# Optimization experiments

Measured on AMD Instinct MI355X. Metric: run time of the kernel, lower is better.

## Reference

```python
import jax, jax.numpy as jnp
import numpy as np

MAP_W = 500
INTERP_H, INTERP_W = 1024, 2048


def _bilinear_ac(x, out_h, out_w):
    # torch F.interpolate(mode='bilinear', align_corners=True), separable
    N, C, H, W = x.shape
    ys = jnp.linspace(0.0, H - 1, out_h)
    y0 = jnp.floor(ys).astype(jnp.int32)
    y1 = jnp.minimum(y0 + 1, H - 1)
    wy = (ys - y0.astype(x.dtype))[None, None, :, None]
    rows = x[:, :, y0, :] * (1 - wy) + x[:, :, y1, :] * wy  # (N,C,out_h,W)
    xs = jnp.linspace(0.0, W - 1, out_w)
    x0 = jnp.floor(xs).astype(jnp.int32)
    x1 = jnp.minimum(x0 + 1, W - 1)
    wx = (xs - x0.astype(x.dtype))[None, None, None, :]
    return rows[:, :, :, x0] * (1 - wx) + rows[:, :, :, x1] * wx


def _conv(x, w, pad):
    return jax.lax.conv_general_dilated(x, w, (1, 1), [(pad, pad), (pad, pad)],
                                        dimension_numbers=('NCHW', 'OIHW', 'NCHW'))


def _bn_relu(x, g, b):
    # BatchNorm2d in training mode: biased batch stats over (N,H,W)
    mu = jnp.mean(x, axis=(0, 2, 3), keepdims=True)
    var = jnp.var(x, axis=(0, 2, 3), keepdims=True)
    xn = (x - mu) * jax.lax.rsqrt(var + 1e-5)
    return jax.nn.relu(xn * g[None, :, None, None] + b[None, :, None, None])


def setup_inputs() -> dict:
    key = jax.random.key(0)
    ks = jax.random.split(key, 24)
    C, NOBJ = 64, 21
    features = jax.random.normal(ks[0], (1, 1, C, 256, 512), dtype=jnp.float32)
    proj_indices = jax.random.randint(ks[1], (1, MAP_W * MAP_W), 0, 400000, dtype=jnp.int64)
    masks_inliers = jax.random.bernoulli(ks[2], 0.5, (1, INTERP_H, INTERP_W))
    rgb_no_norm = jax.random.uniform(ks[3], (1, INTERP_H, INTERP_W, 3), dtype=jnp.float32) * 255.0
    def cw(k, o, i, kh, kw):
        return jax.random.normal(k, (o, i, kh, kw), dtype=jnp.float32) * (1.0 / np.sqrt(i * kh * kw))
    return {
        'features': features, 'proj_indices': proj_indices,
        'masks_inliers': masks_inliers, 'rgb_no_norm': rgb_no_norm,
        'w1': cw(ks[4], 128, C, 7, 7), 'g1': jnp.ones(128), 'b1': jnp.zeros(128),
        'w2': cw(ks[5], 64, 128, 3, 3), 'g2': jnp.ones(64), 'b2': jnp.zeros(64),
        'w3': cw(ks[6], 48, 64, 3, 3), 'g3': jnp.ones(48), 'b3': jnp.zeros(48),
        'w4': cw(ks[7], 48, 48, 3, 3), 'g4': jnp.ones(48), 'b4': jnp.zeros(48),
        'w5': cw(ks[8], NOBJ, 48, 1, 1), 'b5': jnp.zeros(NOBJ),
    }


def reference(features, proj_indices, masks_inliers, rgb_no_norm,
              w1, g1, b1, w2, g2, b2, w3, g3, b3, w4, g4, b4, w5, b5):
    N, T, C, H, W = features.shape  # N = 1
    feat = _bilinear_ac(features[:, 0], INTERP_H, INTERP_W)      # (N,C,1024,2048)
    feat = feat.transpose(0, 2, 3, 1).reshape(-1, C)             # row-major NHWC flatten
    rgb_flat = rgb_no_norm.reshape(-1, 3)
    mask_flat = masks_inliers.reshape(-1)
    # stable compaction: inlier pixels first, in original row-major order
    # (equivalent to torch boolean-mask gather feature[mask_inliers, :])
    order = jnp.argsort((~mask_flat).astype(jnp.int32), stable=True)
    compact_f = feat[order]
    compact_rgb = rgb_flat[order]
    idx = proj_indices.reshape(-1)
    m = idx < jnp.max(idx)                                       # sentinel = max value
    state = jnp.where(m[:, None], compact_f[idx], 0.0)           # replace-mode scatter
    state_rgb = jnp.where(m[:, None], compact_rgb[idx], 0.0)
    rgb_write = state_rgb.reshape(MAP_W, MAP_W, 3)
    observed_masks = m.reshape(N, MAP_W, MAP_W)
    memory = state.reshape(N, MAP_W, MAP_W, C).transpose(0, 3, 1, 2)
    # decoder (first conv in_channels fixed to C to match memory)
    x = _bn_relu(_conv(memory, w1, 3), g1, b1)
    x = _bn_relu(_conv(x, w2, 1), g2, b2)
    x = _bn_relu(_conv(x, w3, 1), g3, b3)
    x = _bn_relu(_conv(x, w4, 1), g4, b4)
    semmap = _conv(x, w5, 0) + b5[None, :, None, None]
    return (semmap, observed_masks, rgb_write)
```

## Files before the change

kernel.cpp:

```cpp
#include <hip/hip_runtime.h>

#define MAPN 250000
#define NPIX 2097152

typedef unsigned short ushort_t;
typedef __attribute__((ext_vector_type(4))) float f32x4;

__device__ inline ushort_t f2bf(float f){
  unsigned u = __float_as_uint(f);
  u = (u + 0x7fffu + ((u >> 16) & 1u)) >> 16;
  return (ushort_t)u;
}
__device__ inline float bf2f(ushort_t h){ return __uint_as_float(((unsigned)h) << 16); }

__device__ __forceinline__ void glds16(const void* g, void* l){
  __builtin_amdgcn_global_load_lds((const __attribute__((address_space(1))) unsigned int*)g,
                                   (__attribute__((address_space(3))) unsigned int*)l, 16, 0, 0);
}

__device__ inline int read_mask(const void* p, int i, int t){
  if (t==0) return ((const int*)p)[i] != 0;
  if (t==1) return ((const unsigned char*)p)[i] != 0;
  if (t==3) return ((const long long*)p)[i] != 0;
  return ((const float*)p)[i] != 0.0f;
}
__device__ inline int read_idx(const void* p, int i, int t){
  if (t==1) return (int)((const long long*)p)[i];
  return ((const int*)p)[i];
}

__global__ void detect_kernel(const int* __restrict__ mask_w, const int* __restrict__ idx_w,
                              int* __restrict__ flags, int* __restrict__ maxidx){
  int tid = threadIdx.x;
  int orv=0, modd=0, inz=0;
  for (int i=tid;i<4096;i+=256) orv |= mask_w[i];
  for (int i=tid;i<2048;i+=256) modd += (mask_w[2*i+1]!=0);
  for (int i=tid;i<2048;i+=256) inz  += (idx_w[2*i+1]!=0);
  __shared__ int sOr[256], sM[256], sI[256];
  sOr[tid]=orv; sM[tid]=modd; sI[tid]=inz; __syncthreads();
  for (int o=128;o;o>>=1){ if(tid<o){ sOr[tid]|=sOr[tid+o]; sM[tid]+=sM[tid+o]; sI[tid]+=sI[tid+o]; } __syncthreads(); }
  if (tid==0){
    int o = sOr[0];
    int mt;
    if ((o & ~1) == 0)               mt = (sM[0] > 0) ? 0 : 3;
    else if ((o & ~0x01010101) == 0) mt = 1;
    else                             mt = 2;
    flags[0] = mt;
    flags[1] = (sI[0] > 0) ? 0 : 1;
    maxidx[0] = 0;
  }
}

__global__ void feat_transpose(const float* __restrict__ f, ushort_t* __restrict__ out){
  __shared__ float tile[64][65];
  int tid = threadIdx.x;
  int y = blockIdx.y;
  int x0 = blockIdx.x * 64;
  #pragma unroll
  for (int pass=0; pass<16; pass++){
    int c = pass*4 + (tid>>6);
    int x = x0 + (tid & 63);
    tile[c][tid & 63] = f[(size_t)c*131072 + (size_t)y*512 + x];
  }
  __syncthreads();
  #pragma unroll
  for (int pass=0; pass<16; pass++){
    int xl = pass*4 + (tid>>6);
    int c  = tid & 63;
    out[((size_t)y*512 + x0 + xl)*64 + c] = f2bf(tile[c][xl]);
  }
}

__global__ void scan_count(const void* __restrict__ mask, const int* __restrict__ flags,
                           int* __restrict__ blkSums){
  int t = flags[0];
  int tid = threadIdx.x;
  int base = blockIdx.x*1024 + tid*4;
  int s = 0;
  #pragma unroll
  for (int j=0;j<4;j++) s += read_mask(mask, base+j, t);
  __shared__ int red[256];
  red[tid] = s; __syncthreads();
  for (int o=128;o;o>>=1){ if (tid<o) red[tid]+=red[tid+o]; __syncthreads(); }
  if (tid==0) blkSums[blockIdx.x] = red[0];
}

__global__ void scan_offsets(const int* __restrict__ blkSums, int* __restrict__ blkOffs){
  __shared__ int tsum[256];
  int tid = threadIdx.x;
  int loc[8]; int s=0;
  #pragma unroll
  for (int j=0;j<8;j++){ loc[j]=blkSums[tid*8+j]; s+=loc[j]; }
  tsum[tid]=s; __syncthreads();
  for (int o=1;o<256;o<<=1){
    int v = (tid>=o)? tsum[tid-o] : 0;
    __syncthreads();
    tsum[tid] += v;
    __syncthreads();
  }
  int run = tsum[tid]-s;
  #pragma unroll
  for (int j=0;j<8;j++){ blkOffs[tid*8+j]=run; run+=loc[j]; }
  if (tid==255) blkOffs[2048]=run;
}

__global__ void build_table(const void* __restrict__ mask, const int* __restrict__ flags,
                            const int* __restrict__ blkOffs, int* __restrict__ table){
  int t = flags[0];
  int tid = threadIdx.x;
  int base = blockIdx.x*1024 + tid*4;
  int mv[4]; int s=0;
  #pragma unroll
  for (int j=0;j<4;j++){ mv[j]=read_mask(mask, base+j, t); s+=mv[j]; }
  __shared__ int red[256];
  red[tid]=s; __syncthreads();
  for (int o=1;o<256;o<<=1){
    int v = (tid>=o)? red[tid-o] : 0;
    __syncthreads();
    red[tid]+=v;
    __syncthreads();
  }
  int excl = red[tid]-s + blkOffs[blockIdx.x];
  int total = blkOffs[2048];
  #pragma unroll
  for (int j=0;j<4;j++){
    int p = base+j;
    int pos;
    if (mv[j]){ pos = excl; excl++; }
    else      { pos = total + (p - excl); }
    table[pos] = p;
  }
}

__global__ void max_idx_kernel(const void* __restrict__ idxp, const int* __restrict__ flags,
                               int* __restrict__ mx){
  int t = flags[1];
  int m = 0;
  for (int i = blockIdx.x*blockDim.x + threadIdx.x; i < MAPN; i += gridDim.x*blockDim.x)
    m = max(m, read_idx(idxp, i, t));
  #pragma unroll
  for (int o=32;o;o>>=1) m = max(m, __shfl_down(m, o));
  if ((threadIdx.x & 63) == 0) atomicMax(mx, m);
}

__global__ void gather_kernel(const void* __restrict__ idxp, const int* __restrict__ flags,
                              const int* __restrict__ mxp, const int* __restrict__ table,
                              const ushort_t* __restrict__ Fhwc, const float* __restrict__ rgb,
                              unsigned char* __restrict__ mem_f8, float* __restrict__ out_obs,
                              float* __restrict__ out_rgb){
  int cell = blockIdx.x*4 + (threadIdx.x>>6);
  int lane = threadIdx.x & 63;
  int t = flags[1];
  int mx = *mxp;
  int idx = read_idx(idxp, cell, t);
  bool m = idx < mx;
  float v = 0.0f, r = 0.0f;
  if (m){
    int p = table[idx];
    int py = p >> 11, px = p & 2047;
    float fy = py * (255.0f/1023.0f);
    int y0 = (int)fy; float wy = fy - (float)y0; int y1 = min(y0+1, 255);
    float fx = px * (511.0f/2047.0f);
    int x0 = (int)fx; float wx = fx - (float)x0; int x1 = min(x0+1, 511);
    const ushort_t* f00 = Fhwc + ((size_t)y0*512 + x0)*64;
    const ushort_t* f01 = Fhwc + ((size_t)y0*512 + x1)*64;
    const ushort_t* f10 = Fhwc + ((size_t)y1*512 + x0)*64;
    const ushort_t* f11 = Fhwc + ((size_t)y1*512 + x1)*64;
    float w00=(1.0f-wy)*(1.0f-wx), w01=(1.0f-wy)*wx, w10=wy*(1.0f-wx), w11=wy*wx;
    v = w00*bf2f(f00[lane]) + w01*bf2f(f01[lane]) + w10*bf2f(f10[lane]) + w11*bf2f(f11[lane]);
    if (lane < 3) r = rgb[(size_t)p*3 + lane];
  }
  int q = __builtin_amdgcn_cvt_pk_fp8_f32(v, 0.0f, 0, false);
  mem_f8[(size_t)cell*64 + lane] = (unsigned char)(q & 0xff);
  if (lane == 0) out_obs[cell] = m ? 1.0f : 0.0f;
  if (lane < 3)  out_rgb[(size_t)cell*3 + lane] = r;
}

__device__ void wprep_body(const float* __restrict__ w, unsigned char* __restrict__ out,
                           int O, int I, int CIPAD, int KK, int co){
  int n = KK*CIPAD;
  int NFS = (O+15)>>4;
  int KC  = CIPAD>>5;
  float mx = 0.f;
  for (int e=threadIdx.x; e<n; e+=256){
    int ci = e % CIPAD;
    if (ci < I){
      int t = e / CIPAD;
      mx = fmaxf(mx, fabsf(w[((size_t)co*I + ci)*KK + t]));
    }
  }
  __shared__ float red[256];
  red[threadIdx.x]=mx; __syncthreads();
  for (int o=128;o;o>>=1){ if(threadIdx.x<o) red[threadIdx.x]=fmaxf(red[threadIdx.x],red[threadIdx.x+o]); __syncthreads(); }
  float m = red[0];
  float sc = (m > 0.f) ? exp2f(floorf(log2f(224.0f/m))) : 1.0f;
  for (int e=threadIdx.x; e<n; e+=256){
    int t = e / CIPAD, ci = e % CIPAD;
    float v = (ci < I) ? w[((size_t)co*I + ci)*KK + t]*sc : 0.0f;
    int q = __builtin_amdgcn_cvt_pk_fp8_f32(v, 0.0f, 0, false);
    int kc = ci>>5, g=(ci>>3)&3, j=ci&7;
    int l = g*16 + (co&15);
    size_t pos = ((size_t)(t*KC + kc)*NFS + (co>>4))*512 + l*8 + j;
    out[pos] = (unsigned char)(q & 0xff);
  }
}

__global__ void wprep_all(const float* __restrict__ w1, unsigned char* __restrict__ o1,
                          const float* __restrict__ w2, unsigned char* __restrict__ o2,
                          const float* __restrict__ w3, unsigned char* __restrict__ o3,
                          const float* __restrict__ w4, unsigned char* __restrict__ o4){
  int b = blockIdx.x;
  if      (b < 128) wprep_body(w1, o1, 128, 64, 64, 49, b);
  else if (b < 192) wprep_body(w2, o2, 64, 128, 128, 9, b-128);
  else if (b < 240) wprep_body(w3, o3, 48, 64, 64, 9, b-192);
  else              wprep_body(w4, o4, 48, 48, 64, 9, b-240);
}

template<int CI, int CO, int COPAD, int KS, int PAD, bool HASBN, int CIREAL,
         int TR, int WM, int WN>
__global__ __launch_bounds__(256, 2) void conv2d_f8(const void* __restrict__ in,
                                                    const unsigned char* __restrict__ wt,
                                                    const float* __restrict__ scsh,
                                                    ushort_t* __restrict__ out,
                                                    float* __restrict__ partials){
  constexpr int TCOL = 64;
  constexpr int ECOL = TCOL + 2*PAD;
  constexpr int E    = TR*ECOL;
  constexpr int MF   = TR*4;
  constexpr int MI   = MF/WM;
  constexpr int NFS  = CO/16;
  constexpr int NFW  = NFS/WN;
  constexpr int KC   = CI/32;
  constexpr int CIG  = CI/8;
  constexpr int TB   = CO*CI;
  constexpr int NSL  = TB/1024;
  constexpr int TOT  = E*CIG;
  constexpr int PASSES = (TOT+255)/256;
  constexpr int SCN = HASBN ? CIREAL : 1;

  __shared__ unsigned char sA[E*CI + 128];
  __shared__ unsigned char sB[KS*TB];
  __shared__ float sStat[4][NFW][16][2];
  __shared__ float sSc[SCN], sSh[SCN];

  const int tid = threadIdx.x, lane = tid & 63, wv = tid >> 6;
  const int wm = wv / WN, wn = wv % WN;
  const int cc = blockIdx.x & 7;
  const int rb = blockIdx.x >> 3;
  const int x0 = cc*TCOL, yb = rb*TR;

  const ushort_t* inb = (const ushort_t*)in;
  const unsigned char* in8 = (const unsigned char*)in;

  if (HASBN){
    for (int i=tid;i<CIREAL;i+=256){ sSc[i]=scsh[i]; sSh[i]=scsh[CIREAL+i]; }
    __syncthreads();
  }

  int ebase[MI], frow[MI], fcolb[MI];
  #pragma unroll
  for (int mi=0;mi<MI;mi++){
    int f = wm*MI + mi;
    frow[mi]  = f >> 2;
    fcolb[mi] = (f & 3) * 16;
    ebase[mi] = frow[mi]*ECOL + fcolb[mi] + (lane & 15);
  }

  f32x4 acc[MI][NFW];
  #pragma unroll
  for (int mi=0;mi<MI;mi++)
    #pragma unroll
    for (int ni=0;ni<NFW;ni++) acc[mi][ni] = (f32x4)0.0f;

  if constexpr (!HASBN){
    uint2 areg[PASSES];
    #pragma unroll
    for (int i=0;i<PASSES;i++){
      int c = i*256 + tid;
      uint2 q = make_uint2(0u,0u);
      if ((TOT % 256 == 0) || c < TOT){
        int e = c / CIG, ci8 = (c % CIG)*8;
        int row = e / ECOL, col = e % ECOL;
        int yy = yb + row - PAD;
        int xx = x0 + col - PAD;
        if (((unsigned)yy < 500u) && ((unsigned)xx < 500u))
          q = *(const uint2*)(in8 + ((size_t)yy*500 + xx)*CI + ci8);
      }
      areg[i] = q;
    }
    for (int kh=0; kh<KS; kh++){
      #pragma unroll
      for (int i=0;i<PASSES;i++){
        int c = i*256 + tid;
        if ((TOT % 256 == 0) || c < TOT){
          int e = c / CIG, ci8 = (c % CIG)*8;
          unsigned wa = ((unsigned)(e*CI + ci8)) ^ ((unsigned)(e&15)<<3);
          *(uint2*)(sA + wa) = areg[i];
        }
      }
      {
        const char* wsrc = (const char*)wt + (size_t)kh*KS*TB;
        for (int s=wv; s<KS*NSL; s+=4)
          glds16(wsrc + (size_t)s*1024 + lane*16, &sB[s*1024]);
      }
      __syncthreads();
      if (kh+1 < KS){
        #pragma unroll
        for (int i=0;i<PASSES;i++){
          int c = i*256 + tid;
          uint2 q = make_uint2(0u,0u);
          if ((TOT % 256 == 0) || c < TOT){
            int e = c / CIG, ci8 = (c % CIG)*8;
            int row = e / ECOL, col = e % ECOL;
            int yy = yb + row + (kh+1) - PAD;
            int xx = x0 + col - PAD;
            if (((unsigned)yy < 500u) && ((unsigned)xx < 500u))
              q = *(const uint2*)(in8 + ((size_t)yy*500 + xx)*CI + ci8);
          }
          areg[i] = q;
        }
      }
      for (int kw=0; kw<KS; kw++){
        const unsigned char* bb = sB + kw*TB;
        #pragma unroll
        for (int kc=0;kc<KC;kc++){
          long long bfr[NFW];
          #pragma unroll
          for (int ni=0;ni<NFW;ni++)
            bfr[ni] = *(const long long*)(bb + (((kc*NFS + wn*NFW + ni)<<9) + lane*8));
          #pragma unroll
          for (int mi=0;mi<MI;mi++){
            int e = ebase[mi] + kw;
            unsigned ra = ((unsigned)(e*CI + kc*32 + (lane>>4)*8)) ^ ((unsigned)(e&15)<<3);
            long long af = *(const long long*)(sA + ra);
            #pragma unroll
            for (int ni=0;ni<NFW;ni++)
              acc[mi][ni] = __builtin_amdgcn_mfma_f32_16x16x32_fp8_fp8(af, bfr[ni], acc[mi][ni], 0,0,0);
          }
        }
      }
      __syncthreads();
    }
  } else {
    for (int kh=0; kh<KS; kh++){
      #pragma unroll
      for (int i=0;i<PASSES;i++){
        int c = i*256 + tid;
        if ((TOT % 256 == 0) || c < TOT){
          int e = c / CIG, ci8 = (c % CIG)*8;
          int row = e / ECOL, col = e % ECOL;
          int yy = yb + row + kh - PAD;
          int xx = x0 + col - PAD;
          uint2 q = make_uint2(0u,0u);
          bool ok = ((unsigned)yy < 500u) && ((unsigned)xx < 500u) && (ci8 < CIREAL);
          if (ok){
            uint4 v = *(const uint4*)(inb + ((size_t)yy*500 + xx)*CI + ci8);
            ushort_t* hv = (ushort_t*)&v;
            float f[8];
            #pragma unroll
            for (int j=0;j<8;j++)
              f[j] = fmaxf(fmaf(bf2f(hv[j]), sSc[ci8+j], sSh[ci8+j]), 0.0f);
            int d0 = __builtin_amdgcn_cvt_pk_fp8_f32(f[0], f[1], 0, false);
            d0     = __builtin_amdgcn_cvt_pk_fp8_f32(f[2], f[3], d0, true);
            int d1 = __builtin_amdgcn_cvt_pk_fp8_f32(f[4], f[5], 0, false);
            d1     = __builtin_amdgcn_cvt_pk_fp8_f32(f[6], f[7], d1, true);
            q = make_uint2((unsigned)d0, (unsigned)d1);
          }
          unsigned wa = ((unsigned)(e*CI + ci8)) ^ ((unsigned)(e&15)<<3);
          *(uint2*)(sA + wa) = q;
        }
      }
      {
        const char* wsrc = (const char*)wt + (size_t)kh*KS*TB;
        for (int s=wv; s<KS*NSL; s+=4)
          glds16(wsrc + (size_t)s*1024 + lane*16, &sB[s*1024]);
      }
      __syncthreads();

      for (int kw=0; kw<KS; kw++){
        const unsigned char* bb = sB + kw*TB;
        #pragma unroll
        for (int kc=0;kc<KC;kc++){
          long long bfr[NFW];
          #pragma unroll
          for (int ni=0;ni<NFW;ni++)
            bfr[ni] = *(const long long*)(bb + (((kc*NFS + wn*NFW + ni)<<9) + lane*8));
          #pragma unroll
          for (int mi=0;mi<MI;mi++){
            int e = ebase[mi] + kw;
            unsigned ra = ((unsigned)(e*CI + kc*32 + (lane>>4)*8)) ^ ((unsigned)(e&15)<<3);
            long long af = *(const long long*)(sA + ra);
            #pragma unroll
            for (int ni=0;ni<NFW;ni++)
              acc[mi][ni] = __builtin_amdgcn_mfma_f32_16x16x32_fp8_fp8(af, bfr[ni], acc[mi][ni], 0,0,0);
          }
        }
      }
      __syncthreads();
    }
  }

  #pragma unroll
  for (int ni=0;ni<NFW;ni++){
    float ps=0.f, pq=0.f;
    #pragma unroll
    for (int mi=0;mi<MI;mi++){
      int colb = fcolb[mi] + (lane>>4)*4;
      size_t rowoff = (size_t)(yb + frow[mi])*500;
      #pragma unroll
      for (int j=0;j<4;j++){
        float v = acc[mi][ni][j];
        int colAbs = x0 + colb + j;
        if (colAbs < 500){
          ps += v; pq += v*v;
          out[(rowoff + colAbs)*COPAD + wn*(NFW*16) + ni*16 + (lane&15)] = f2bf(v);
        }
      }
    }
    ps += __shfl_xor(ps, 16); pq += __shfl_xor(pq, 16);
    ps += __shfl_xor(ps, 32); pq += __shfl_xor(pq, 32);
    if (lane < 16){ sStat[wv][ni][lane][0]=ps; sStat[wv][ni][lane][1]=pq; }
  }
  __syncthreads();
  if (tid < CO){
    int wn_ = tid / (NFW*16);
    int r = tid % (NFW*16);
    int ni_ = r >> 4, col = r & 15;
    float s = 0.f, q = 0.f;
    #pragma unroll
    for (int m=0;m<WM;m++){
      s += sStat[m*WN + wn_][ni_][col][0];
      q += sStat[m*WN + wn_][ni_][col][1];
    }
    partials[(size_t)blockIdx.x*(2*CO) + tid]      = s;
    partials[(size_t)blockIdx.x*(2*CO) + CO + tid] = q;
  }
}

__global__ void bn_reduce2(const float* __restrict__ partials, int nblk, int CO,
                           const float* __restrict__ g, const float* __restrict__ b,
                           float* __restrict__ scsh){
  int c = blockIdx.x;
  float s=0.f, q=0.f;
  for (int i=threadIdx.x; i<nblk; i+=256){
    s += partials[(size_t)i*(2*CO) + c];
    q += partials[(size_t)i*(2*CO) + CO + c];
  }
  __shared__ float rs[256], rq[256];
  rs[threadIdx.x]=s; rq[threadIdx.x]=q; __syncthreads();
  for (int o=128;o;o>>=1){
    if (threadIdx.x<o){ rs[threadIdx.x]+=rs[threadIdx.x+o]; rq[threadIdx.x]+=rq[threadIdx.x+o]; }
    __syncthreads();
  }
  if (threadIdx.x==0){
    float mean = rs[0]*(1.0f/(float)MAPN);
    float var  = rq[0]*(1.0f/(float)MAPN) - mean*mean;
    float inv  = rsqrtf(var + 1e-5f);
    float sc   = g[c]*inv;
    scsh[c]    = sc;
    scsh[CO+c] = b[c] - mean*sc;
  }
}

__global__ void conv5_kernel(const ushort_t* __restrict__ in, const float* __restrict__ w,
                             const float* __restrict__ bias, const float* __restrict__ scsh,
                             float* __restrict__ out){
  __shared__ float sw[21*48];
  __shared__ float sb[21];
  __shared__ float sc[48], sh[48];
  for (int i=threadIdx.x;i<1008;i+=256) sw[i]=w[i];
  if (threadIdx.x<21) sb[threadIdx.x]=bias[threadIdx.x];
  if (threadIdx.x<48){ sc[threadIdx.x]=scsh[threadIdx.x]; sh[threadIdx.x]=scsh[48+threadIdx.x]; }
  __syncthreads();
  int pix = blockIdx.x*256 + threadIdx.x;
  if (pix >= MAPN) return;
  float acc[21];
  #pragma unroll
  for (int i=0;i<21;i++) acc[i]=0.0f;
  const ushort_t* ip = in + (size_t)pix*64;
  #pragma unroll
  for (int cg=0; cg<6; cg++){
    uint4 v = *(const uint4*)(ip + cg*8);
    ushort_t* hv = (ushort_t*)&v;
    #pragma unroll
    for (int j=0;j<8;j++){
      int ci = cg*8+j;
      float s = fmaxf(fmaf(bf2f(hv[j]), sc[ci], sh[ci]), 0.0f);
      #pragma unroll
      for (int co=0;co<21;co++) acc[co]=fmaf(s, sw[co*48+ci], acc[co]);
    }
  }
  #pragma unroll
  for (int co=0;co<21;co++) out[(size_t)co*MAPN + pix] = acc[co] + sb[co];
}

static inline size_t al256(size_t x){ return (x + 255) & ~(size_t)255; }

extern "C" void kernel_launch(void* const* d_in, const int* in_sizes, int n_in,
                              void* d_out, int out_size, void* d_ws, size_t ws_size,
                              hipStream_t stream){
  const float* features = (const float*)d_in[0];
  const void*  proj     = d_in[1];
  const void*  mask     = d_in[2];
  const float* rgb      = (const float*)d_in[3];
  const float* w1 = (const float*)d_in[4];
  const float* g1 = (const float*)d_in[5];
  const float* b1 = (const float*)d_in[6];
  const float* w2 = (const float*)d_in[7];
  const float* g2 = (const float*)d_in[8];
  const float* b2 = (const float*)d_in[9];
  const float* w3 = (const float*)d_in[10];
  const float* g3 = (const float*)d_in[11];
  const float* b3 = (const float*)d_in[12];
  const float* w4 = (const float*)d_in[13];
  const float* g4 = (const float*)d_in[14];
  const float* b4 = (const float*)d_in[15];
  const float* w5 = (const float*)d_in[16];
  const float* b5 = (const float*)d_in[17];

  char* ws = (char*)d_ws;
  size_t off = 0;
  unsigned char* mem_f8 = (unsigned char*)(ws + off); off += al256((size_t)MAPN*64);
  ushort_t* actA   = (ushort_t*)(ws + off); off += al256((size_t)MAPN*128*2);
  ushort_t* actB   = (ushort_t*)(ws + off); off += al256((size_t)MAPN*64*2);
  ushort_t* Fhwc   = (ushort_t*)(ws + off); off += al256((size_t)131072*64*2);
  int*      table  = (int*)(ws + off);      off += al256((size_t)NPIX*4);
  unsigned char* wh1 = (unsigned char*)(ws + off); off += al256((size_t)49*64*128);
  unsigned char* wh2 = (unsigned char*)(ws + off); off += al256((size_t)9*128*64);
  unsigned char* wh3 = (unsigned char*)(ws + off); off += al256((size_t)9*64*48);
  unsigned char* wh4 = (unsigned char*)(ws + off); off += al256((size_t)9*64*48);
  float*    partials = (float*)(ws + off);  off += al256((size_t)2048*256*4);
  int* blkSums = (int*)(ws + off); off += al256(2048*4);
  int* blkOffs = (int*)(ws + off); off += al256(2049*4);
  int* maxidx  = (int*)(ws + off); off += 256;
  int* flags   = (int*)(ws + off); off += 256;
  float* scsh1 = (float*)(ws + off); off += al256(256*4);
  float* scsh2 = (float*)(ws + off); off += al256(256*4);
  float* scsh3 = (float*)(ws + off); off += al256(256*4);
  float* scsh4 = (float*)(ws + off); off += al256(256*4);

  float* out_sem = (float*)d_out;
  float* out_obs = out_sem + (size_t)21*MAPN;
  float* out_rgb = out_obs + MAPN;

  detect_kernel<<<1,256,0,stream>>>((const int*)mask, (const int*)proj, flags, maxidx);
  feat_transpose<<<dim3(8,256),256,0,stream>>>(features, Fhwc);

  scan_count<<<2048,256,0,stream>>>(mask, flags, blkSums);
  scan_offsets<<<1,256,0,stream>>>(blkSums, blkOffs);
  build_table<<<2048,256,0,stream>>>(mask, flags, blkOffs, table);

  max_idx_kernel<<<256,256,0,stream>>>(proj, flags, maxidx);

  wprep_all<<<288,256,0,stream>>>(w1, wh1, w2, wh2, w3, wh3, w4, wh4);

  gather_kernel<<<62500,256,0,stream>>>(proj, flags, maxidx, table, Fhwc, rgb,
                                        mem_f8, out_obs, out_rgb);

  conv2d_f8<64,128,128,7,3,false,64,4,2,2><<<125*8,256,0,stream>>>(mem_f8, wh1, nullptr, actA, partials);
  bn_reduce2<<<128,256,0,stream>>>(partials, 1000, 128, g1, b1, scsh1);

  conv2d_f8<128,64,64,3,1,true,128,4,2,2><<<125*8,256,0,stream>>>(actA, wh2, scsh1, actB, partials);
  bn_reduce2<<<64,256,0,stream>>>(partials, 1000, 64, g2, b2, scsh2);

  conv2d_f8<64,48,64,3,1,true,64,4,4,1><<<125*8,256,0,stream>>>(actB, wh3, scsh2, actA, partials);
  bn_reduce2<<<48,256,0,stream>>>(partials, 1000, 48, g3, b3, scsh3);

  conv2d_f8<64,48,64,3,1,true,48,4,4,1><<<125*8,256,0,stream>>>(actA, wh4, scsh3, actB, partials);
  bn_reduce2<<<48,256,0,stream>>>(partials, 1000, 48, g4, b4, scsh4);

  conv5_kernel<<<(MAPN+255)/256,256,0,stream>>>(actB, w5, b5, scsh4, out_sem);
}
```

Before: 422.2 us.

## Use 16x16x128 scaled MFMA for 7x7 conv1 with split output channels

Replaces the generic fp8 conv for the first 7x7 layer with a dedicated kernel using the larger-K mfma_scale 16x16x128 f8f6f4 instruction. Pairs of kw taps are packed into the 128-wide K dimension, with zero padding for the odd tap, and the weights are re-laid out by a new prep kernel. Output channels are split across a second grid dimension (2x64), which doubles the block count and shrinks per-block weight shared memory. The costs are one wasted zero-padded K slice per row and a new BN partial-reduction kernel matching the split layout.

New measurement: 946.7 us. 124% more time.

```diff
diff --git a/kernel.cpp b/kernel.cpp
--- a/kernel.cpp
+++ b/kernel.cpp
@@ -5,6 +5,9 @@
 
 typedef unsigned short ushort_t;
 typedef __attribute__((ext_vector_type(4))) float f32x4;
+typedef __attribute__((ext_vector_type(8))) int int8v;
+
+union U8 { long long q[4]; int8v v; };
 
 __device__ inline ushort_t f2bf(float f){
   unsigned u = __float_as_uint(f);
@@ -176,6 +179,37 @@
   if (lane < 3)  out_rgb[(size_t)cell*3 + lane] = r;
 }
 
+__global__ void wprep1_mx(const float* __restrict__ w, unsigned char* __restrict__ out){
+  int co = blockIdx.x;
+  float mx = 0.f;
+  for (int e=threadIdx.x; e<3136; e+=256){
+    int ci = e & 63, t = e >> 6;
+    mx = fmaxf(mx, fabsf(w[((size_t)co*64 + ci)*49 + t]));
+  }
+  __shared__ float red[256];
+  red[threadIdx.x]=mx; __syncthreads();
+  for (int o=128;o;o>>=1){ if(threadIdx.x<o) red[threadIdx.x]=fmaxf(red[threadIdx.x],red[threadIdx.x+o]); __syncthreads(); }
+  float m = red[0];
+  float sc = (m > 0.f) ? exp2f(floorf(log2f(224.0f/m))) : 1.0f;
+  int nf = co>>4, zz = nf>>2, nfz = nf&3;
+  for (int e=threadIdx.x; e<3136; e+=256){
+    int ci = e & 63, t = e >> 6;
+    int kh = t/7, kw = t - kh*7;
+    float v = w[((size_t)co*64 + ci)*49 + t]*sc;
+    int q = __builtin_amdgcn_cvt_pk_fp8_f32(v, 0.0f, 0, false);
+    int p = kw>>1, k = ((kw&1)<<6) | ci;
+    int ln = (k>>5)*16 + (co&15), j = k&31;
+    size_t pos = ((size_t)((kh*2 + zz)*4 + p)*4 + nfz)*2048 + (j>>3)*512 + ln*8 + (j&7);
+    out[pos] = (unsigned char)(q & 0xff);
+  }
+  for (int e=threadIdx.x; e<448; e+=256){
+    int kh = e>>6; int k = 64 + (e&63);
+    int ln = (k>>5)*16 + (co&15), j = k&31;
+    size_t pos = ((size_t)((kh*2 + zz)*4 + 3)*4 + nfz)*2048 + (j>>3)*512 + ln*8 + (j&7);
+    out[pos] = 0;
+  }
+}
+
 __device__ void wprep_body(const float* __restrict__ w, unsigned char* __restrict__ out,
                            int O, int I, int CIPAD, int KK, int co){
   int n = KK*CIPAD;
@@ -205,19 +239,181 @@
   }
 }
 
-__global__ void wprep_all(const float* __restrict__ w1, unsigned char* __restrict__ o1,
-                          const float* __restrict__ w2, unsigned char* __restrict__ o2,
+__global__ void wprep_all(const float* __restrict__ w2, unsigned char* __restrict__ o2,
                           const float* __restrict__ w3, unsigned char* __restrict__ o3,
                           const float* __restrict__ w4, unsigned char* __restrict__ o4){
   int b = blockIdx.x;
-  if      (b < 128) wprep_body(w1, o1, 128, 64, 64, 49, b);
-  else if (b < 192) wprep_body(w2, o2, 64, 128, 128, 9, b-128);
-  else if (b < 240) wprep_body(w3, o3, 48, 64, 64, 9, b-192);
-  else              wprep_body(w4, o4, 48, 48, 64, 9, b-240);
-}
-
-template<int CI, int CO, int COPAD, int KS, int PAD, bool HASBN, int CIREAL,
-         int TR, int WM, int WN>
+  if      (b < 64)  wprep_body(w2, o2, 64, 128, 128, 9, b);
+  else if (b < 112) wprep_body(w3, o3, 48, 64, 64, 9, b-64);
+  else              wprep_body(w4, o4, 48, 48, 64, 9, b-112);
+}
+
+__global__ __launch_bounds__(256, 2) void conv1_mx(const unsigned char* __restrict__ in8,
+                                                   const unsigned char* __restrict__ wt,
+                                                   ushort_t* __restrict__ out,
+                                                   float* __restrict__ partials){
+  constexpr int ECOL = 70, E = 280, CIG = 8, TOT = E*CIG, PASSES = 9;
+  __shared__ unsigned char sA[E*64 + 128];
+  __shared__ unsigned char sB[32768];
+  __shared__ float sStat[4][2][16][2];
+
+  const int tid = threadIdx.x, lane = tid & 63, wv = tid >> 6;
+  const int wm = wv >> 1, wn = wv & 1;
+  const int cc = blockIdx.x & 7, rb = blockIdx.x >> 3;
+  const int z = blockIdx.y;
+  const int x0 = cc*64, yb = rb*4;
+
+  int ebase[8], frow[8], fcolb[8];
+  #pragma unroll
+  for (int mi=0;mi<8;mi++){
+    int f = wm*8 + mi;
+    frow[mi]  = f >> 2;
+    fcolb[mi] = (f & 3) * 16;
+    ebase[mi] = frow[mi]*ECOL + fcolb[mi] + (lane & 15);
+  }
+
+  f32x4 acc[8][2];
+  #pragma unroll
+  for (int mi=0;mi<8;mi++){ acc[mi][0]=(f32x4)0.0f; acc[mi][1]=(f32x4)0.0f; }
+
+  uint2 areg[PASSES];
+  #pragma unroll
+  for (int i=0;i<PASSES;i++){
+    int c = i*256 + tid;
+    uint2 q = make_uint2(0u,0u);
+    if (c < TOT){
+      int e = c / CIG, ci8 = (c % CIG)*8;
+      int row = e / ECOL, col = e % ECOL;
+      int yy = yb + row - 3, xx = x0 + col - 3;
+      if (((unsigned)yy < 500u) && ((unsigned)xx < 500u))
+        q = *(const uint2*)(in8 + ((size_t)yy*500 + xx)*64 + ci8);
+    }
+    areg[i] = q;
+  }
+
+  for (int kh=0; kh<7; kh++){
+    #pragma unroll
+    for (int i=0;i<PASSES;i++){
+      int c = i*256 + tid;
+      if (c < TOT){
+        int e = c / CIG, ci8 = (c % CIG)*8;
+        unsigned wa = ((unsigned)(e*64 + ci8)) ^ ((unsigned)(e&15)<<3);
+        *(uint2*)(sA + wa) = areg[i];
+      }
+    }
+    {
+      const char* wsrc = (const char*)wt + (size_t)(kh*2 + z)*32768;
+      for (int s=wv; s<32; s+=4)
+        glds16(wsrc + (size_t)s*1024 + lane*16, &sB[s*1024]);
+    }
+    __syncthreads();
+    if (kh+1 < 7){
+      #pragma unroll
+      for (int i=0;i<PASSES;i++){
+        int c = i*256 + tid;
+        uint2 q = make_uint2(0u,0u);
+        if (c < TOT){
+          int e = c / CIG, ci8 = (c % CIG)*8;
+          int row = e / ECOL, col = e % ECOL;
+          int yy = yb + row + (kh+1) - 3, xx = x0 + col - 3;
+          if (((unsigned)yy < 500u) && ((unsigned)xx < 500u))
+            q = *(const uint2*)(in8 + ((size_t)yy*500 + xx)*64 + ci8);
+        }
+        areg[i] = q;
+      }
+    }
+    #pragma unroll
+    for (int p=0;p<4;p++){
+      U8 b0, b1;
+      {
+        unsigned bb0 = (unsigned)((p*4 + wn*2 + 0)*2048) + lane*8;
+        unsigned bb1 = (unsigned)((p*4 + wn*2 + 1)*2048) + lane*8;
+        b0.q[0]=*(const long long*)(sB+bb0);      b0.q[1]=*(const long long*)(sB+bb0+512);
+        b0.q[2]=*(const long long*)(sB+bb0+1024); b0.q[3]=*(const long long*)(sB+bb0+1536);
+        b1.q[0]=*(const long long*)(sB+bb1);      b1.q[1]=*(const long long*)(sB+bb1+512);
+        b1.q[2]=*(const long long*)(sB+bb1+1024); b1.q[3]=*(const long long*)(sB+bb1+1536);
+      }
+      #pragma unroll
+      for (int mi=0;mi<8;mi++){
+        int e = ebase[mi] + 2*p + ((lane>>5)&1);
+        unsigned ab = (unsigned)(e*64 + ((lane>>4)&1)*32);
+        unsigned sw = (unsigned)((e&15)<<3);
+        U8 a;
+        a.q[0]=*(const long long*)(sA + ((ab   )^sw));
+        a.q[1]=*(const long long*)(sA + ((ab+ 8)^sw));
+        a.q[2]=*(const long long*)(sA + ((ab+16)^sw));
+        a.q[3]=*(const long long*)(sA + ((ab+24)^sw));
+        acc[mi][0] = __builtin_amdgcn_mfma_scale_f32_16x16x128_f8f6f4(
+                       a.v, b0.v, acc[mi][0], 0, 0, 0, 0x7f7f7f7f, 0, 0x7f7f7f7f);
+        acc[mi][1] = __builtin_amdgcn_mfma_scale_f32_16x16x128_f8f6f4(
+                       a.v, b1.v, acc[mi][1], 0, 0, 0, 0x7f7f7f7f, 0, 0x7f7f7f7f);
+      }
+    }
+    __syncthreads();
+  }
+
+  #pragma unroll
+  for (int ni=0;ni<2;ni++){
+    float ps=0.f, pq=0.f;
+    #pragma unroll
+    for (int mi=0;mi<8;mi++){
+      int colb = fcolb[mi] + (lane>>4)*4;
+      size_t rowoff = (size_t)(yb + frow[mi])*500;
+      #pragma unroll
+      for (int j=0;j<4;j++){
+        float v = acc[mi][ni][j];
+        int colAbs = x0 + colb + j;
+        if (colAbs < 500){
+          ps += v; pq += v*v;
+          out[(rowoff + colAbs)*128 + z*64 + wn*32 + ni*16 + (lane&15)] = f2bf(v);
+        }
+      }
+    }
+    ps += __shfl_xor(ps, 16); pq += __shfl_xor(pq, 16);
+    ps += __shfl_xor(ps, 32); pq += __shfl_xor(pq, 32);
+    if (lane < 16){ sStat[wv][ni][lane][0]=ps; sStat[wv][ni][lane][1]=pq; }
+  }
+  __syncthreads();
+  if (tid < 64){
+    int wn_ = tid >> 5;
+    int r = tid & 31;
+    int ni_ = r >> 4, col = r & 15;
+    float s = sStat[0*2+wn_][ni_][col][0] + sStat[1*2+wn_][ni_][col][0];
+    float q = sStat[0*2+wn_][ni_][col][1] + sStat[1*2+wn_][ni_][col][1];
+    size_t row = (size_t)z*1000 + blockIdx.x;
+    partials[row*128 + tid]      = s;
+    partials[row*128 + 64 + tid] = q;
+  }
+}
+
+__global__ void bn_reduce_l1(const float* __restrict__ partials,
+                             const float* __restrict__ g, const float* __restrict__ b,
+                             float* __restrict__ scsh){
+  int c = blockIdx.x;
+  int zz = c >> 6, cc = c & 63;
+  const float* base = partials + (size_t)zz*1000*128;
+  float s=0.f, q=0.f;
+  for (int i=threadIdx.x; i<1000; i+=256){
+    s += base[(size_t)i*128 + cc];
+    q += base[(size_t)i*128 + 64 + cc];
+  }
+  __shared__ float rs[256], rq[256];
+  rs[threadIdx.x]=s; rq[threadIdx.x]=q; __syncthreads();
+  for (int o=128;o;o>>=1){
+    if (threadIdx.x<o){ rs[threadIdx.x]+=rs[threadIdx.x+o]; rq[threadIdx.x]+=rq[threadIdx.x+o]; }
+    __syncthreads();
+  }
+  if (threadIdx.x==0){
+    float mean = rs[0]*(1.0f/(float)MAPN);
+    float var  = rq[0]*(1.0f/(float)MAPN) - mean*mean;
+    float inv  = rsqrtf(var + 1e-5f);
+    float sc   = g[c]*inv;
+    scsh[c]     = sc;
+    scsh[128+c] = b[c] - mean*sc;
+  }
+}
+
+template<int CI, int CO, int COPAD, int KS, int PAD, int CIREAL, int TR, int WM, int WN>
 __global__ __launch_bounds__(256, 2) void conv2d_f8(const void* __restrict__ in,
                                                     const unsigned char* __restrict__ wt,
                                                     const float* __restrict__ scsh,
@@ -236,12 +432,11 @@
   constexpr int NSL  = TB/1024;
   constexpr int TOT  = E*CIG;
   constexpr int PASSES = (TOT+255)/256;
-  constexpr int SCN = HASBN ? CIREAL : 1;
 
   __shared__ unsigned char sA[E*CI + 128];
   __shared__ unsigned char sB[KS*TB];
   __shared__ float sStat[4][NFW][16][2];
-  __shared__ float sSc[SCN], sSh[SCN];
+  __shared__ float sSc[CIREAL], sSh[CIREAL];
 
   const int tid = threadIdx.x, lane = tid & 63, wv = tid >> 6;
   const int wm = wv / WN, wn = wv % WN;
@@ -250,12 +445,9 @@
   const int x0 = cc*TCOL, yb = rb*TR;
 
   const ushort_t* inb = (const ushort_t*)in;
-  const unsigned char* in8 = (const unsigned char*)in;
-
-  if (HASBN){
-    for (int i=tid;i<CIREAL;i+=256){ sSc[i]=scsh[i]; sSh[i]=scsh[CIREAL+i]; }
-    __syncthreads();
-  }
+
+  for (int i=tid;i<CIREAL;i+=256){ sSc[i]=scsh[i]; sSh[i]=scsh[CIREAL+i]; }
+  __syncthreads();
 
   int ebase[MI], frow[MI], fcolb[MI];
   #pragma unroll
@@ -272,132 +464,61 @@
     #pragma unroll
     for (int ni=0;ni<NFW;ni++) acc[mi][ni] = (f32x4)0.0f;
 
-  if constexpr (!HASBN){
-    uint2 areg[PASSES];
+  for (int kh=0; kh<KS; kh++){
     #pragma unroll
     for (int i=0;i<PASSES;i++){
       int c = i*256 + tid;
-      uint2 q = make_uint2(0u,0u);
       if ((TOT % 256 == 0) || c < TOT){
         int e = c / CIG, ci8 = (c % CIG)*8;
         int row = e / ECOL, col = e % ECOL;
-        int yy = yb + row - PAD;
+        int yy = yb + row + kh - PAD;
         int xx = x0 + col - PAD;
-        if (((unsigned)yy < 500u) && ((unsigned)xx < 500u))
-          q = *(const uint2*)(in8 + ((size_t)yy*500 + xx)*CI + ci8);
-      }
-      areg[i] = q;
-    }
-    for (int kh=0; kh<KS; kh++){
+        uint2 q = make_uint2(0u,0u);
+        bool ok = ((unsigned)yy < 500u) && ((unsigned)xx < 500u) && (ci8 < CIREAL);
+        if (ok){
+          uint4 v = *(const uint4*)(inb + ((size_t)yy*500 + xx)*CI + ci8);
+          ushort_t* hv = (ushort_t*)&v;
+          float f[8];
+          #pragma unroll
+          for (int j=0;j<8;j++)
+            f[j] = fmaxf(fmaf(bf2f(hv[j]), sSc[ci8+j], sSh[ci8+j]), 0.0f);
+          int d0 = __builtin_amdgcn_cvt_pk_fp8_f32(f[0], f[1], 0, false);
+          d0     = __builtin_amdgcn_cvt_pk_fp8_f32(f[2], f[3], d0, true);
+          int d1 = __builtin_amdgcn_cvt_pk_fp8_f32(f[4], f[5], 0, false);
+          d1     = __builtin_amdgcn_cvt_pk_fp8_f32(f[6], f[7], d1, true);
+          q = make_uint2((unsigned)d0, (unsigned)d1);
+        }
+        unsigned wa = ((unsigned)(e*CI + ci8)) ^ ((unsigned)(e&15)<<3);
+        *(uint2*)(sA + wa) = q;
+      }
+    }
+    {
+      const char* wsrc = (const char*)wt + (size_t)kh*KS*TB;
+      for (int s=wv; s<KS*NSL; s+=4)
+        glds16(wsrc + (size_t)s*1024 + lane*16, &sB[s*1024]);
+    }
+    __syncthreads();
+
+    for (int kw=0; kw<KS; kw++){
+      const unsigned char* bb = sB + kw*TB;
       #pragma unroll
-      for (int i=0;i<PASSES;i++){
-        int c = i*256 + tid;
-        if ((TOT % 256 == 0) || c < TOT){
-          int e = c / CIG, ci8 = (c % CIG)*8;
-          unsigned wa = ((unsigned)(e*CI + ci8)) ^ ((unsigned)(e&15)<<3);
-          *(uint2*)(sA + wa) = areg[i];
-        }
-      }
-      {
-        const char* wsrc = (const char*)wt + (size_t)kh*KS*TB;
-        for (int s=wv; s<KS*NSL; s+=4)
-          glds16(wsrc + (size_t)s*1024 + lane*16, &sB[s*1024]);
-      }
-      __syncthreads();
-      if (kh+1 < KS){
+      for (int kc=0;kc<KC;kc++){
+        long long bfr[NFW];
         #pragma unroll
-        for (int i=0;i<PASSES;i++){
-          int c = i*256 + tid;
-          uint2 q = make_uint2(0u,0u);
-          if ((TOT % 256 == 0) || c < TOT){
-            int e = c / CIG, ci8 = (c % CIG)*8;
-            int row = e / ECOL, col = e % ECOL;
-            int yy = yb + row + (kh+1) - PAD;
-            int xx = x0 + col - PAD;
-            if (((unsigned)yy < 500u) && ((unsigned)xx < 500u))
-              q = *(const uint2*)(in8 + ((size_t)yy*500 + xx)*CI + ci8);
-          }
-          areg[i] = q;
-        }
-      }
-      for (int kw=0; kw<KS; kw++){
-        const unsigned char* bb = sB + kw*TB;
+        for (int ni=0;ni<NFW;ni++)
+          bfr[ni] = *(const long long*)(bb + (((kc*NFS + wn*NFW + ni)<<9) + lane*8));
         #pragma unroll
-        for (int kc=0;kc<KC;kc++){
-          long long bfr[NFW];
+        for (int mi=0;mi<MI;mi++){
+          int e = ebase[mi] + kw;
+          unsigned ra = ((unsigned)(e*CI + kc*32 + (lane>>4)*8)) ^ ((unsigned)(e&15)<<3);
+          long long af = *(const long long*)(sA + ra);
           #pragma unroll
           for (int ni=0;ni<NFW;ni++)
-            bfr[ni] = *(const long long*)(bb + (((kc*NFS + wn*NFW + ni)<<9) + lane*8));
-          #pragma unroll
-          for (int mi=0;mi<MI;mi++){
-            int e = ebase[mi] + kw;
-            unsigned ra = ((unsigned)(e*CI + kc*32 + (lane>>4)*8)) ^ ((unsigned)(e&15)<<3);
-            long long af = *(const long long*)(sA + ra);
-            #pragma unroll
-            for (int ni=0;ni<NFW;ni++)
-              acc[mi][ni] = __builtin_amdgcn_mfma_f32_16x16x32_fp8_fp8(af, bfr[ni], acc[mi][ni], 0,0,0);
-          }
+            acc[mi][ni] = __builtin_amdgcn_mfma_f32_16x16x32_fp8_fp8(af, bfr[ni], acc[mi][ni], 0,0,0);
         }
       }
-      __syncthreads();
-    }
-  } else {
-    for (int kh=0; kh<KS; kh++){
-      #pragma unroll
-      for (int i=0;i<PASSES;i++){
-        int c = i*256 + tid;
-        if ((TOT % 256 == 0) || c < TOT){
-          int e = c / CIG, ci8 = (c % CIG)*8;
-          int row = e / ECOL, col = e % ECOL;
-          int yy = yb + row + kh - PAD;
-          int xx = x0 + col - PAD;
-          uint2 q = make_uint2(0u,0u);
-          bool ok = ((unsigned)yy < 500u) && ((unsigned)xx < 500u) && (ci8 < CIREAL);
-          if (ok){
-            uint4 v = *(const uint4*)(inb + ((size_t)yy*500 + xx)*CI + ci8);
-            ushort_t* hv = (ushort_t*)&v;
-            float f[8];
-            #pragma unroll
-            for (int j=0;j<8;j++)
-              f[j] = fmaxf(fmaf(bf2f(hv[j]), sSc[ci8+j], sSh[ci8+j]), 0.0f);
-            int d0 = __builtin_amdgcn_cvt_pk_fp8_f32(f[0], f[1], 0, false);
-            d0     = __builtin_amdgcn_cvt_pk_fp8_f32(f[2], f[3], d0, true);
-            int d1 = __builtin_amdgcn_cvt_pk_fp8_f32(f[4], f[5], 0, false);
-            d1     = __builtin_amdgcn_cvt_pk_fp8_f32(f[6], f[7], d1, true);
-            q = make_uint2((unsigned)d0, (unsigned)d1);
-          }
-          unsigned wa = ((unsigned)(e*CI + ci8)) ^ ((unsigned)(e&15)<<3);
-          *(uint2*)(sA + wa) = q;
-        }
-      }
-      {
-        const char* wsrc = (const char*)wt + (size_t)kh*KS*TB;
-        for (int s=wv; s<KS*NSL; s+=4)
-          glds16(wsrc + (size_t)s*1024 + lane*16, &sB[s*1024]);
-      }
-      __syncthreads();
-
-      for (int kw=0; kw<KS; kw++){
-        const unsigned char* bb = sB + kw*TB;
-        #pragma unroll
-        for (int kc=0;kc<KC;kc++){
-          long long bfr[NFW];
-          #pragma unroll
-          for (int ni=0;ni<NFW;ni++)
-            bfr[ni] = *(const long long*)(bb + (((kc*NFS + wn*NFW + ni)<<9) + lane*8));
-          #pragma unroll
-          for (int mi=0;mi<MI;mi++){
-            int e = ebase[mi] + kw;
-            unsigned ra = ((unsigned)(e*CI + kc*32 + (lane>>4)*8)) ^ ((unsigned)(e&15)<<3);
-            long long af = *(const long long*)(sA + ra);
-            #pragma unroll
-            for (int ni=0;ni<NFW;ni++)
-              acc[mi][ni] = __builtin_amdgcn_mfma_f32_16x16x32_fp8_fp8(af, bfr[ni], acc[mi][ni], 0,0,0);
-          }
-        }
-      }
-      __syncthreads();
-    }
+    }
+    __syncthreads();
   }
 
   #pragma unroll
@@ -525,7 +646,7 @@
   ushort_t* actB   = (ushort_t*)(ws + off); off += al256((size_t)MAPN*64*2);
   ushort_t* Fhwc   = (ushort_t*)(ws + off); off += al256((size_t)131072*64*2);
   int*      table  = (int*)(ws + off);      off += al256((size_t)NPIX*4);
-  unsigned char* wh1 = (unsigned char*)(ws + off); off += al256((size_t)49*64*128);
+  unsigned char* wh1 = (unsigned char*)(ws + off); off += al256((size_t)7*2*32768);
   unsigned char* wh2 = (unsigned char*)(ws + off); off += al256((size_t)9*128*64);
   unsigned char* wh3 = (unsigned char*)(ws + off); off += al256((size_t)9*64*48);
   unsigned char* wh4 = (unsigned char*)(ws + off); off += al256((size_t)9*64*48);
@@ -552,21 +673,22 @@
 
   max_idx_kernel<<<256,256,0,stream>>>(proj, flags, maxidx);
 
-  wprep_all<<<288,256,0,stream>>>(w1, wh1, w2, wh2, w3, wh3, w4, wh4);
+  wprep1_mx<<<128,256,0,stream>>>(w1, wh1);
+  wprep_all<<<160,256,0,stream>>>(w2, wh2, w3, wh3, w4, wh4);
 
   gather_kernel<<<62500,256,0,stream>>>(proj, flags, maxidx, table, Fhwc, rgb,
                                         mem_f8, out_obs, out_rgb);
 
-  conv2d_f8<64,128,128,7,3,false,64,4,2,2><<<125*8,256,0,stream>>>(mem_f8, wh1, nullptr, actA, partials);
-  bn_reduce2<<<128,256,0,stream>>>(partials, 1000, 128, g1, b1, scsh1);
-
-  conv2d_f8<128,64,64,3,1,true,128,4,2,2><<<125*8,256,0,stream>>>(actA, wh2, scsh1, actB, partials);
+  conv1_mx<<<dim3(1000,2),256,0,stream>>>(mem_f8, wh1, actA, partials);
+  bn_reduce_l1<<<128,256,0,stream>>>(partials, g1, b1, scsh1);
+
+  conv2d_f8<128,64,64,3,1,128,4,2,2><<<125*8,256,0,stream>>>(actA, wh2, scsh1, actB, partials);
   bn_reduce2<<<64,256,0,stream>>>(partials, 1000, 64, g2, b2, scsh2);
 
-  conv2d_f8<64,48,64,3,1,true,64,4,4,1><<<125*8,256,0,stream>>>(actB, wh3, scsh2, actA, partials);
+  conv2d_f8<64,48,64,3,1,64,4,4,1><<<125*8,256,0,stream>>>(actB, wh3, scsh2, actA, partials);
   bn_reduce2<<<48,256,0,stream>>>(partials, 1000, 48, g3, b3, scsh3);
 
-  conv2d_f8<64,48,64,3,1,true,48,4,4,1><<<125*8,256,0,stream>>>(actA, wh4, scsh3, actB, partials);
+  conv2d_f8<64,48,64,3,1,48,4,4,1><<<125*8,256,0,stream>>>(actA, wh4, scsh3, actB, partials);
   bn_reduce2<<<48,256,0,stream>>>(partials, 1000, 48, g4, b4, scsh4);
 
   conv5_kernel<<<(MAPN+255)/256,256,0,stream>>>(actB, w5, b5, scsh4, out_sem);
```
